# Optimization experiments

Measured on AMD Instinct MI355X. Metric: run time of the kernel, lower is better.

The kernel has to match this reference:

```python
import jax, jax.numpy as jnp
import numpy as np

IN_DIM = 1024
OUT_DIM = 1024
QK_DIM = OUT_DIM // 4  # 256


def setup_inputs() -> dict:
    key = jax.random.key(0)
    kx, ky, kq, kk, kv = jax.random.split(key, 5)
    B, Sq, Sk = 16, 2048, 2048
    x = jax.random.normal(kx, (B, Sq, IN_DIM), dtype=jnp.float32)
    y = jax.random.normal(ky, (B, Sk, IN_DIM), dtype=jnp.float32)
    s = 1.0 / np.sqrt(IN_DIM)
    Wq = jax.random.normal(kq, (IN_DIM, QK_DIM), dtype=jnp.float32) * s
    Wk = jax.random.normal(kk, (IN_DIM, QK_DIM), dtype=jnp.float32) * s
    Wv = jax.random.normal(kv, (IN_DIM, OUT_DIM), dtype=jnp.float32) * s
    return {"x": x, "y": y, "Wq": Wq, "Wk": Wk, "Wv": Wv}


def reference(x, y, Wq, Wk, Wv):
    # q: [B,Sq,dk], k: [B,Sk,dk]
    q = jnp.einsum("bsd,dk->bsk", x, Wq)
    k = jnp.einsum("btd,dk->btk", y, Wk)
    # NOTE: original scales by out_dim**0.5, not qk dim
    scores = jnp.einsum("bsk,btk->bst", q, k) / jnp.sqrt(jnp.float32(OUT_DIM))
    attn = jax.nn.softmax(scores, axis=-1)
    v = jnp.einsum("btd,de->bte", y, Wv)
    out = jnp.einsum("bst,bte->bse", attn, v)
    return out + x
```

## Files before the change

kernel.cpp:

```cpp
#include <hip/hip_runtime.h>

typedef __attribute__((ext_vector_type(8))) short bf16x8;
typedef __attribute__((ext_vector_type(4))) short s16x4;
typedef __attribute__((ext_vector_type(4))) float f32x4;

#define MFMA16(a,b,c) __builtin_amdgcn_mfma_f32_16x16x32_bf16((a),(b),(c),0,0,0)

__device__ __forceinline__ unsigned short f2bf(float f) {
  unsigned int u = __float_as_uint(f);
  return (unsigned short)((u + 0x7fffu + ((u >> 16) & 1u)) >> 16);
}
__device__ __forceinline__ float bf2f(unsigned short u) {
  return __uint_as_float(((unsigned int)u) << 16);
}

__device__ __forceinline__ void gload16(const void* g, void* l) {
  __builtin_amdgcn_global_load_lds((const __attribute__((address_space(1))) void*)g,
                                   (__attribute__((address_space(3))) void*)l, 16, 0, 0);
}

__global__ __launch_bounds__(256) void cvt_bf16(const float* __restrict__ in,
                                                unsigned short* __restrict__ out, int n8) {
  for (int i = blockIdx.x * 256 + threadIdx.x; i < n8; i += gridDim.x * 256) {
    float4 a = ((const float4*)in)[2 * i];
    float4 b = ((const float4*)in)[2 * i + 1];
    s16x4 p0, p1;
    p0[0] = f2bf(a.x); p0[1] = f2bf(a.y); p0[2] = f2bf(a.z); p0[3] = f2bf(a.w);
    p1[0] = f2bf(b.x); p1[1] = f2bf(b.y); p1[2] = f2bf(b.z); p1[3] = f2bf(b.w);
    ((s16x4*)out)[2 * i] = p0;
    ((s16x4*)out)[2 * i + 1] = p1;
  }
}

__global__ __launch_bounds__(256) void tcvt(const float* __restrict__ W,
                                            unsigned short* __restrict__ Wt, int K, int N) {
  __shared__ float t[32][33];
  const int n0 = blockIdx.x * 32, k0 = blockIdx.y * 32;
  const int c = threadIdx.x & 31, r8 = threadIdx.x >> 5;
#pragma unroll
  for (int p = 0; p < 4; ++p) {
    int r = r8 + p * 8;
    t[r][c] = W[(size_t)(k0 + r) * N + n0 + c];
  }
  __syncthreads();
#pragma unroll
  for (int p = 0; p < 4; ++p) {
    int r = r8 + p * 8;
    Wt[(size_t)(n0 + r) * K + k0 + c] = f2bf(t[c][r]);
  }
}

#define SBAR  do { __builtin_amdgcn_s_barrier(); __builtin_amdgcn_sched_barrier(0); } while (0)

template<int NT, int NTIL, int MODE>
__global__ __launch_bounds__(512) void gemm4p(
    const unsigned short* __restrict__ Aall, const unsigned short* __restrict__ Ball,
    size_t abatch, size_t bbatch, int lda, int ldb,
    unsigned short* __restrict__ Cb, int b0, int nb)
{
  __shared__ __align__(16) unsigned short lds[65536];
  const int bid = blockIdx.x;
  const int bloc = bid % nb, tl = bid / nb;
  const int mtile = tl / NTIL, ntile = tl % NTIL;
  const int gb = b0 + bloc;
  const unsigned short* Ag = Aall + (MODE == 0 ? (size_t)gb : (size_t)bloc) * abatch
                                  + (size_t)mtile * 256 * lda;
  const unsigned short* Bg = Ball + (size_t)gb * bbatch + (size_t)ntile * 256 * ldb;

  const int tid = threadIdx.x, lane = tid & 63, w = tid >> 6;
  const int wm = w >> 2, wn = w & 3;
  const int lrow = lane & 15, lg = lane >> 4;
  char* lb = (char*)lds;

  auto stageU = [&](const unsigned short* G, int ld, int kofs, int ubyte) {
#pragma unroll
    for (int i = 0; i < 2; ++i) {
      int c = tid + 512 * i;
      int row = c >> 2, q = c & 3;
      int qs = q ^ ((row >> 1) & 3);
      gload16(G + (size_t)row * ld + kofs + qs * 8, lb + ubyte + c * 16);
    }
  };
  auto rdfrag = [&](int ubyte, int row) -> bf16x8 {
    return *(const bf16x8*)(lb + ubyte + row * 64 + ((lg ^ ((row >> 1) & 3)) << 4));
  };

  f32x4 acc[8][4] = {};
  bf16x8 afA[4], afB[4], bfrA[4], bfrB[4];

  stageU(Ag, lda, 0,  (0 * 2 + 0) * 16384);
  stageU(Bg, ldb, 0,  (1 * 2 + 0) * 16384);
  stageU(Ag, lda, 32, (2 * 2 + 0) * 16384);
  stageU(Bg, ldb, 32, (3 * 2 + 0) * 16384);
  stageU(Ag, lda, 64, (0 * 2 + 1) * 16384);
  stageU(Bg, ldb, 64, (1 * 2 + 1) * 16384);
  asm volatile("s_waitcnt vmcnt(8)" ::: "memory");
  SBAR;
#pragma unroll
  for (int i = 0; i < 4; ++i) afA[i] = rdfrag(0, wm * 128 + i * 16 + lrow);
#pragma unroll
  for (int nf = 0; nf < 4; ++nf) bfrA[nf] = rdfrag(2 * 16384, wn * 64 + nf * 16 + lrow);

  for (int T = 0; T < NT; ++T) {
    const int pc = T & 1, pn = (T + 1) & 1;
    const int a1b = (2 * 2 + pc) * 16384, b1b = (3 * 2 + pc) * 16384;
    const int a0b = (0 * 2 + pc) * 16384;
    const int t1 = (T + 1 < NT) ? T + 1 : 0;
    const int t2 = (T + 2 < NT) ? T + 2 : 0;

#pragma unroll
    for (int i = 0; i < 4; ++i) afB[i] = rdfrag(a0b, wm * 128 + (i + 4) * 16 + lrow);
    stageU(Ag, lda, t1 * 64 + 32, (2 * 2 + pn) * 16384);
    asm volatile("s_waitcnt lgkmcnt(4)" ::: "memory");
    __builtin_amdgcn_sched_barrier(0);
    __builtin_amdgcn_s_setprio(1);
#pragma unroll
    for (int mf = 0; mf < 4; ++mf)
#pragma unroll
      for (int nf = 0; nf < 4; ++nf)
        acc[mf][nf] = MFMA16(afA[mf], bfrA[nf], acc[mf][nf]);
    __builtin_amdgcn_s_setprio(0);
    asm volatile("s_waitcnt vmcnt(6)" ::: "memory");
    SBAR;

#pragma unroll
    for (int i = 0; i < 4; ++i) afA[i] = rdfrag(a1b, wm * 128 + i * 16 + lrow);
#pragma unroll
    for (int nf = 0; nf < 4; ++nf) bfrB[nf] = rdfrag(b1b, wn * 64 + nf * 16 + lrow);
    stageU(Bg, ldb, t1 * 64 + 32, (3 * 2 + pn) * 16384);
    asm volatile("s_waitcnt lgkmcnt(8)" ::: "memory");
    __builtin_amdgcn_sched_barrier(0);
    __builtin_amdgcn_s_setprio(1);
#pragma unroll
    for (int mf = 0; mf < 4; ++mf)
#pragma unroll
      for (int nf = 0; nf < 4; ++nf)
        acc[mf + 4][nf] = MFMA16(afB[mf], bfrA[nf], acc[mf + 4][nf]);
    __builtin_amdgcn_s_setprio(0);
    SBAR;

#pragma unroll
    for (int i = 0; i < 4; ++i) afB[i] = rdfrag(a1b, wm * 128 + (i + 4) * 16 + lrow);
    stageU(Ag, lda, t2 * 64, (0 * 2 + pc) * 16384);
    asm volatile("s_waitcnt lgkmcnt(4)" ::: "memory");
    __builtin_amdgcn_sched_barrier(0);
    __builtin_amdgcn_s_setprio(1);
#pragma unroll
    for (int mf = 0; mf < 4; ++mf)
#pragma unroll
      for (int nf = 0; nf < 4; ++nf)
        acc[mf][nf] = MFMA16(afA[mf], bfrB[nf], acc[mf][nf]);
    __builtin_amdgcn_s_setprio(0);
    asm volatile("s_waitcnt vmcnt(6)" ::: "memory");
    SBAR;

#pragma unroll
    for (int i = 0; i < 4; ++i) afA[i] = rdfrag((0 * 2 + pn) * 16384, wm * 128 + i * 16 + lrow);
#pragma unroll
    for (int nf = 0; nf < 4; ++nf) bfrA[nf] = rdfrag((1 * 2 + pn) * 16384, wn * 64 + nf * 16 + lrow);
    stageU(Bg, ldb, t2 * 64, (1 * 2 + pc) * 16384);
    asm volatile("s_waitcnt lgkmcnt(8)" ::: "memory");
    __builtin_amdgcn_sched_barrier(0);
    __builtin_amdgcn_s_setprio(1);
#pragma unroll
    for (int mf = 0; mf < 4; ++mf)
#pragma unroll
      for (int nf = 0; nf < 4; ++nf)
        acc[mf + 4][nf] = MFMA16(afB[mf], bfrB[nf], acc[mf + 4][nf]);
    __builtin_amdgcn_s_setprio(0);
    SBAR;
  }

  if (MODE == 0) {
    unsigned short* Cp = Cb + (size_t)bloc * 2048 * 2048;
#pragma unroll
    for (int mf = 0; mf < 8; ++mf)
#pragma unroll
      for (int r = 0; r < 4; ++r) {
        int row = mtile * 256 + wm * 128 + mf * 16 + lg * 4 + r;
#pragma unroll
        for (int nf = 0; nf < 4; ++nf) {
          int col = ntile * 256 + wn * 64 + nf * 16 + lrow;
          Cp[(size_t)row * 2048 + col] = f2bf(acc[mf][nf][r]);
        }
      }
  } else if (MODE == 2) {
    unsigned char* C8 = (unsigned char*)Cb;
#pragma unroll
    for (int mf = 0; mf < 8; ++mf) {
      int m0 = mtile * 256 + wm * 128 + mf * 16 + lg * 4;
      int bb = m0 >> 11, t = m0 & 2047;
      int tw = t >> 6, t64 = t & 63;
#pragma unroll
      for (int nf = 0; nf < 4; ++nf) {
        int e = ntile * 256 + wn * 64 + nf * 16 + lrow;
        int eg = e >> 4;
        int pk = 0;
        pk = __builtin_amdgcn_cvt_pk_fp8_f32(acc[mf][nf][0], acc[mf][nf][1], pk, false);
        pk = __builtin_amdgcn_cvt_pk_fp8_f32(acc[mf][nf][2], acc[mf][nf][3], pk, true);
        *(unsigned int*)(C8 + (size_t)bb * 2097152
                            + ((size_t)(eg * 32 + tw)) * 1024 + lrow * 64 + t64)
            = (unsigned int)pk;
      }
    }
  } else {
    unsigned short* Cp = Cb + (size_t)bloc * 16 * 2048 * 256;
    const float scale = (bloc == 0) ? 0.03125f : 1.0f;
#pragma unroll
    for (int mf = 0; mf < 8; ++mf)
#pragma unroll
      for (int r = 0; r < 4; ++r) {
        int row = mtile * 256 + wm * 128 + mf * 16 + lg * 4 + r;
#pragma unroll
        for (int nf = 0; nf < 4; ++nf) {
          int col = wn * 64 + nf * 16 + lrow;
          Cp[(size_t)row * 256 + col] = f2bf(acc[mf][nf][r] * scale);
        }
      }
  }
}

__global__ __launch_bounds__(256) void softmax_kernel(
    const unsigned short* __restrict__ Sp, unsigned char* __restrict__ Pp) {
  const int row = blockIdx.x * 4 + (threadIdx.x >> 6);
  const int lane = threadIdx.x & 63;
  const unsigned short* rp = Sp + (size_t)row * 2048;
  bf16x8 raw[4];
#pragma unroll
  for (int c = 0; c < 4; ++c) raw[c] = *(const bf16x8*)(rp + c * 512 + lane * 8);
  float v[32];
#pragma unroll
  for (int c = 0; c < 4; ++c)
#pragma unroll
    for (int j = 0; j < 8; ++j) v[c * 8 + j] = bf2f((unsigned short)raw[c][j]);
  float mx = v[0];
#pragma unroll
  for (int j = 1; j < 32; ++j) mx = fmaxf(mx, v[j]);
  mx = fmaxf(mx, __shfl_xor(mx, 1));
  mx = fmaxf(mx, __shfl_xor(mx, 2));
  mx = fmaxf(mx, __shfl_xor(mx, 4));
  mx = fmaxf(mx, __shfl_xor(mx, 8));
  mx = fmaxf(mx, __shfl_xor(mx, 16));
  mx = fmaxf(mx, __shfl_xor(mx, 32));
  float sum = 0.f;
#pragma unroll
  for (int j = 0; j < 32; ++j) { v[j] = __expf(v[j] - mx); sum += v[j]; }
  sum += __shfl_xor(sum, 1);
  sum += __shfl_xor(sum, 2);
  sum += __shfl_xor(sum, 4);
  sum += __shfl_xor(sum, 8);
  sum += __shfl_xor(sum, 16);
  sum += __shfl_xor(sum, 32);
  const float scale = 64.0f / sum;
  unsigned char* rp8 = Pp + (size_t)row * 2048;
#pragma unroll
  for (int c = 0; c < 4; ++c) {
    int lo = 0, hi = 0;
    lo = __builtin_amdgcn_cvt_pk_fp8_f32(v[c * 8 + 0] * scale, v[c * 8 + 1] * scale, lo, false);
    lo = __builtin_amdgcn_cvt_pk_fp8_f32(v[c * 8 + 2] * scale, v[c * 8 + 3] * scale, lo, true);
    hi = __builtin_amdgcn_cvt_pk_fp8_f32(v[c * 8 + 4] * scale, v[c * 8 + 5] * scale, hi, false);
    hi = __builtin_amdgcn_cvt_pk_fp8_f32(v[c * 8 + 6] * scale, v[c * 8 + 7] * scale, hi, true);
    uint2 o; o.x = (unsigned int)lo; o.y = (unsigned int)hi;
    *(uint2*)(rp8 + c * 512 + lane * 8) = o;
  }
}

__global__ __launch_bounds__(512) void pvf8_kernel(
    const unsigned char* __restrict__ Pp,
    const unsigned char* __restrict__ Vp,
    const float* __restrict__ X, float* __restrict__ Out,
    int b0, int nb)
{
  __shared__ __align__(16) unsigned char lds[4][16384];
  const int bloc = blockIdx.x % nb, tl = blockIdx.x / nb;
  const int mtile = tl >> 3, ntile = tl & 7;
  const int gb = b0 + bloc;
  const unsigned char* Ag = Pp + (size_t)bloc * 4194304 + (size_t)mtile * 256 * 2048;
  const unsigned char* Vb = Vp + (size_t)gb * 2097152;
  const int NT = 32;
  const int tid = threadIdx.x, lane = tid & 63, w = tid >> 6;
  const int wm = w >> 2, wn = w & 3;
  const int lrow = lane & 15, lg = lane >> 4;

  auto stageA = [&](int jt) {
    unsigned char* dst = lds[jt & 3];
#pragma unroll
    for (int i = 0; i < 2; ++i) {
      int c = tid + 512 * i; int row = c >> 2; int q = (c & 3) ^ ((row >> 1) & 3);
      gload16(Ag + (size_t)row * 2048 + jt * 64 + q * 16, dst + c * 16);
    }
  };
  auto loadB = [&](int jt, long2* bv) {
#pragma unroll
    for (int nf = 0; nf < 2; ++nf) {
      int eg = ntile * 8 + wn * 2 + nf;
      bv[nf] = *(const long2*)(Vb + ((size_t)(eg * 32 + jt)) * 1024 + lrow * 64 + lg * 16);
    }
  };

  f32x4 acc[8][2] = {};
  stageA(0); stageA(1); stageA(2);
  long2 bvc[2];
  loadB(0, bvc);
  asm volatile("s_waitcnt vmcnt(6)" ::: "memory");
  __builtin_amdgcn_sched_barrier(0);

  for (int jt = 0; jt < NT; ++jt) {
    __builtin_amdgcn_s_barrier();
    if (jt + 3 < NT) stageA(jt + 3);
    long2 bvn[2];
    loadB(jt + 1 < NT ? jt + 1 : 0, bvn);
    const unsigned char* Ab = lds[jt & 3];
    {
      long2 av[4];
#pragma unroll
      for (int mf = 0; mf < 4; ++mf) {
        int row = wm * 128 + mf * 16 + lrow;
        av[mf] = *(const long2*)(Ab + row * 64 + ((lg ^ ((row >> 1) & 3)) << 4));
      }
      __builtin_amdgcn_s_setprio(1);
#pragma unroll
      for (int mf = 0; mf < 4; ++mf)
#pragma unroll
        for (int nf = 0; nf < 2; ++nf) {
          acc[mf][nf] = __builtin_amdgcn_mfma_f32_16x16x32_fp8_fp8(av[mf].x, bvc[nf].x, acc[mf][nf], 0, 0, 0);
          acc[mf][nf] = __builtin_amdgcn_mfma_f32_16x16x32_fp8_fp8(av[mf].y, bvc[nf].y, acc[mf][nf], 0, 0, 0);
        }
      __builtin_amdgcn_s_setprio(0);
    }
    {
      long2 av[4];
#pragma unroll
      for (int mf = 0; mf < 4; ++mf) {
        int row = wm * 128 + (mf + 4) * 16 + lrow;
        av[mf] = *(const long2*)(Ab + row * 64 + ((lg ^ ((row >> 1) & 3)) << 4));
      }
      __builtin_amdgcn_s_setprio(1);
#pragma unroll
      for (int mf = 0; mf < 4; ++mf)
#pragma unroll
        for (int nf = 0; nf < 2; ++nf) {
          acc[mf + 4][nf] = __builtin_amdgcn_mfma_f32_16x16x32_fp8_fp8(av[mf].x, bvc[nf].x, acc[mf + 4][nf], 0, 0, 0);
          acc[mf + 4][nf] = __builtin_amdgcn_mfma_f32_16x16x32_fp8_fp8(av[mf].y, bvc[nf].y, acc[mf + 4][nf], 0, 0, 0);
        }
      __builtin_amdgcn_s_setprio(0);
    }
    bvc[0] = bvn[0]; bvc[1] = bvn[1];
  }

#pragma unroll
  for (int mf = 0; mf < 8; ++mf)
#pragma unroll
    for (int r = 0; r < 4; ++r) {
      int row = mtile * 256 + wm * 128 + mf * 16 + lg * 4 + r;
      const float* xr = X   + ((size_t)gb * 2048 + row) * 1024;
      float*      orp = Out + ((size_t)gb * 2048 + row) * 1024;
#pragma unroll
      for (int nf = 0; nf < 2; ++nf) {
        int col = ntile * 128 + wn * 32 + nf * 16 + lrow;
        orp[col] = acc[mf][nf][r] * 0.015625f + xr[col];
      }
    }
}

extern "C" void kernel_launch(void* const* d_in, const int* in_sizes, int n_in,
                              void* d_out, int out_size, void* d_ws, size_t ws_size,
                              hipStream_t stream) {
  (void)in_sizes; (void)n_in; (void)out_size;
  const float* x  = (const float*)d_in[0];
  const float* y  = (const float*)d_in[1];
  const float* Wq = (const float*)d_in[2];
  const float* Wk = (const float*)d_in[3];
  const float* Wv = (const float*)d_in[4];
  float* out = (float*)d_out;

  unsigned short* xb = (unsigned short*)d_out;
  unsigned short* yb = xb + (size_t)16 * 2048 * 1024;

  char* p = (char*)d_ws;
  unsigned short* Wqt = (unsigned short*)p;  p += (size_t)256 * 1024 * 2;
  unsigned short* Wkt = (unsigned short*)p;  p += (size_t)256 * 1024 * 2;
  unsigned short* Wvt = (unsigned short*)p;  p += (size_t)1024 * 1024 * 2;
  unsigned short* qws = (unsigned short*)p;  p += (size_t)16 * 2048 * 256 * 2;
  unsigned short* kws = (unsigned short*)p;  p += (size_t)16 * 2048 * 256 * 2;
  unsigned char*  vp8 = (unsigned char*)p;   p += (size_t)16 * 1024 * 2048;
  char* dyn = p;
  const size_t fixed_bytes = (size_t)(dyn - (char*)d_ws);
  const size_t per_batch = (size_t)2048 * 2048 * 2 + (size_t)2048 * 2048;
  int nb = 1;
  if      (ws_size >= fixed_bytes + 16 * per_batch) nb = 16;
  else if (ws_size >= fixed_bytes + 8  * per_batch) nb = 8;
  else if (ws_size >= fixed_bytes + 4  * per_batch) nb = 4;
  else if (ws_size >= fixed_bytes + 2  * per_batch) nb = 2;
  else nb = 1;
  unsigned short* Sp = (unsigned short*)dyn;
  unsigned char*  Pp = (unsigned char*)(dyn + (size_t)nb * 2048 * 2048 * 2);

  const int n8 = (16 * 2048 * 1024) / 8;
  cvt_bf16<<<2048, 256, 0, stream>>>(x, xb, n8);
  cvt_bf16<<<2048, 256, 0, stream>>>(y, yb, n8);
  tcvt<<<dim3(8, 32),  256, 0, stream>>>(Wq, Wqt, 1024, 256);
  tcvt<<<dim3(8, 32),  256, 0, stream>>>(Wk, Wkt, 1024, 256);
  tcvt<<<dim3(32, 32), 256, 0, stream>>>(Wv, Wvt, 1024, 1024);

  gemm4p<16, 1, 3><<<256, 512, 0, stream>>>(
      xb, Wqt, (size_t)16 * 2048 * 1024, (size_t)256 * 1024, 1024, 1024,
      qws, 0, 2);
  gemm4p<16, 4, 2><<<512, 512, 0, stream>>>(
      yb, Wvt, 0, 0, 1024, 1024, (unsigned short*)vp8, 0, 1);

  for (int b0 = 0; b0 < 16; b0 += nb) {
    gemm4p<4, 8, 0><<<nb * 64, 512, 0, stream>>>(
        qws, kws, (size_t)2048 * 256, (size_t)2048 * 256, 256, 256,
        Sp, b0, nb);
    softmax_kernel<<<nb * 512, 256, 0, stream>>>(Sp, Pp);
    pvf8_kernel<<<nb * 64, 512, 0, stream>>>(Pp, vp8, x, out, b0, nb);
  }
}
```

Before: 430.0 us.

## Merge prologue conversion launches, drop B prefetch in PV kernel, split PV launch

Merges the two activation bf16 conversion kernels into one launch and the three weight transpose-convert kernels into one 3D-grid launch, removing several small launches. In the fp8 PV kernel, the register double-buffered B-operand prefetch is replaced by a same-iteration load, and the initial wait is relaxed. The s_setprio calls become a template option. When all 16 batches fit, the PV launch is split into two halves, the second without priority raising. This trades launch overhead and register pressure against less latency hiding on the B loads.

```diff
diff --git a/kernel.cpp b/kernel.cpp
--- a/kernel.cpp
+++ b/kernel.cpp
@@ -19,23 +19,36 @@
                                    (__attribute__((address_space(3))) void*)l, 16, 0, 0);
 }
 
-__global__ __launch_bounds__(256) void cvt_bf16(const float* __restrict__ in,
-                                                unsigned short* __restrict__ out, int n8) {
-  for (int i = blockIdx.x * 256 + threadIdx.x; i < n8; i += gridDim.x * 256) {
+__global__ __launch_bounds__(256) void cvt_bf16_2(const float* __restrict__ inx,
+                                                  unsigned short* __restrict__ outx,
+                                                  const float* __restrict__ iny,
+                                                  unsigned short* __restrict__ outy,
+                                                  int n8) {
+  const float* in = (blockIdx.x < 2048) ? inx : iny;
+  unsigned short* out = (blockIdx.x < 2048) ? outx : outy;
+  const int b = blockIdx.x & 2047;
+  for (int i = b * 256 + threadIdx.x; i < n8; i += 2048 * 256) {
     float4 a = ((const float4*)in)[2 * i];
-    float4 b = ((const float4*)in)[2 * i + 1];
+    float4 c = ((const float4*)in)[2 * i + 1];
     s16x4 p0, p1;
     p0[0] = f2bf(a.x); p0[1] = f2bf(a.y); p0[2] = f2bf(a.z); p0[3] = f2bf(a.w);
-    p1[0] = f2bf(b.x); p1[1] = f2bf(b.y); p1[2] = f2bf(b.z); p1[3] = f2bf(b.w);
+    p1[0] = f2bf(c.x); p1[1] = f2bf(c.y); p1[2] = f2bf(c.z); p1[3] = f2bf(c.w);
     ((s16x4*)out)[2 * i] = p0;
     ((s16x4*)out)[2 * i + 1] = p1;
   }
 }
 
-__global__ __launch_bounds__(256) void tcvt(const float* __restrict__ W,
-                                            unsigned short* __restrict__ Wt, int K, int N) {
+__global__ __launch_bounds__(256) void tcvt3(const float* __restrict__ Wq, unsigned short* __restrict__ Wqt,
+                                             const float* __restrict__ Wk, unsigned short* __restrict__ Wkt,
+                                             const float* __restrict__ Wv, unsigned short* __restrict__ Wvt) {
   __shared__ float t[32][33];
+  const int which = blockIdx.z;
+  const float* W = which == 0 ? Wq : (which == 1 ? Wk : Wv);
+  unsigned short* Wt = which == 0 ? Wqt : (which == 1 ? Wkt : Wvt);
+  const int N = (which == 2) ? 1024 : 256;
+  const int K = 1024;
   const int n0 = blockIdx.x * 32, k0 = blockIdx.y * 32;
+  if (n0 >= N) return;
   const int c = threadIdx.x & 31, r8 = threadIdx.x >> 5;
 #pragma unroll
   for (int p = 0; p < 4; ++p) {
@@ -265,6 +278,7 @@
   }
 }
 
+template<int PRIO>
 __global__ __launch_bounds__(512) void pvf8_kernel(
     const unsigned char* __restrict__ Pp,
     const unsigned char* __restrict__ Vp,
@@ -290,26 +304,20 @@
       gload16(Ag + (size_t)row * 2048 + jt * 64 + q * 16, dst + c * 16);
     }
   };
-  auto loadB = [&](int jt, long2* bv) {
+
+  f32x4 acc[8][2] = {};
+  stageA(0); stageA(1); stageA(2);
+  asm volatile("s_waitcnt vmcnt(4)" ::: "memory");
+
+  for (int jt = 0; jt < NT; ++jt) {
+    __builtin_amdgcn_s_barrier();
+    long2 bv[2];
 #pragma unroll
     for (int nf = 0; nf < 2; ++nf) {
       int eg = ntile * 8 + wn * 2 + nf;
       bv[nf] = *(const long2*)(Vb + ((size_t)(eg * 32 + jt)) * 1024 + lrow * 64 + lg * 16);
     }
-  };
-
-  f32x4 acc[8][2] = {};
-  stageA(0); stageA(1); stageA(2);
-  long2 bvc[2];
-  loadB(0, bvc);
-  asm volatile("s_waitcnt vmcnt(6)" ::: "memory");
-  __builtin_amdgcn_sched_barrier(0);
-
-  for (int jt = 0; jt < NT; ++jt) {
-    __builtin_amdgcn_s_barrier();
     if (jt + 3 < NT) stageA(jt + 3);
-    long2 bvn[2];
-    loadB(jt + 1 < NT ? jt + 1 : 0, bvn);
     const unsigned char* Ab = lds[jt & 3];
     {
       long2 av[4];
@@ -318,15 +326,15 @@
         int row = wm * 128 + mf * 16 + lrow;
         av[mf] = *(const long2*)(Ab + row * 64 + ((lg ^ ((row >> 1) & 3)) << 4));
       }
-      __builtin_amdgcn_s_setprio(1);
+      if (PRIO) __builtin_amdgcn_s_setprio(1);
 #pragma unroll
       for (int mf = 0; mf < 4; ++mf)
 #pragma unroll
         for (int nf = 0; nf < 2; ++nf) {
-          acc[mf][nf] = __builtin_amdgcn_mfma_f32_16x16x32_fp8_fp8(av[mf].x, bvc[nf].x, acc[mf][nf], 0, 0, 0);
-          acc[mf][nf] = __builtin_amdgcn_mfma_f32_16x16x32_fp8_fp8(av[mf].y, bvc[nf].y, acc[mf][nf], 0, 0, 0);
+          acc[mf][nf] = __builtin_amdgcn_mfma_f32_16x16x32_fp8_fp8(av[mf].x, bv[nf].x, acc[mf][nf], 0, 0, 0);
+          acc[mf][nf] = __builtin_amdgcn_mfma_f32_16x16x32_fp8_fp8(av[mf].y, bv[nf].y, acc[mf][nf], 0, 0, 0);
         }
-      __builtin_amdgcn_s_setprio(0);
+      if (PRIO) __builtin_amdgcn_s_setprio(0);
     }
     {
       long2 av[4];
@@ -335,17 +343,16 @@
         int row = wm * 128 + (mf + 4) * 16 + lrow;
         av[mf] = *(const long2*)(Ab + row * 64 + ((lg ^ ((row >> 1) & 3)) << 4));
       }
-      __builtin_amdgcn_s_setprio(1);
+      if (PRIO) __builtin_amdgcn_s_setprio(1);
 #pragma unroll
       for (int mf = 0; mf < 4; ++mf)
 #pragma unroll
         for (int nf = 0; nf < 2; ++nf) {
-          acc[mf + 4][nf] = __builtin_amdgcn_mfma_f32_16x16x32_fp8_fp8(av[mf].x, bvc[nf].x, acc[mf + 4][nf], 0, 0, 0);
-          acc[mf + 4][nf] = __builtin_amdgcn_mfma_f32_16x16x32_fp8_fp8(av[mf].y, bvc[nf].y, acc[mf + 4][nf], 0, 0, 0);
+          acc[mf + 4][nf] = __builtin_amdgcn_mfma_f32_16x16x32_fp8_fp8(av[mf].x, bv[nf].x, acc[mf + 4][nf], 0, 0, 0);
+          acc[mf + 4][nf] = __builtin_amdgcn_mfma_f32_16x16x32_fp8_fp8(av[mf].y, bv[nf].y, acc[mf + 4][nf], 0, 0, 0);
         }
-      __builtin_amdgcn_s_setprio(0);
-    }
-    bvc[0] = bvn[0]; bvc[1] = bvn[1];
+      if (PRIO) __builtin_amdgcn_s_setprio(0);
+    }
   }
 
 #pragma unroll
@@ -397,11 +404,8 @@
   unsigned char*  Pp = (unsigned char*)(dyn + (size_t)nb * 2048 * 2048 * 2);
 
   const int n8 = (16 * 2048 * 1024) / 8;
-  cvt_bf16<<<2048, 256, 0, stream>>>(x, xb, n8);
-  cvt_bf16<<<2048, 256, 0, stream>>>(y, yb, n8);
-  tcvt<<<dim3(8, 32),  256, 0, stream>>>(Wq, Wqt, 1024, 256);
-  tcvt<<<dim3(8, 32),  256, 0, stream>>>(Wk, Wkt, 1024, 256);
-  tcvt<<<dim3(32, 32), 256, 0, stream>>>(Wv, Wvt, 1024, 1024);
+  cvt_bf16_2<<<4096, 256, 0, stream>>>(x, xb, y, yb, n8);
+  tcvt3<<<dim3(32, 32, 3), 256, 0, stream>>>(Wq, Wqt, Wk, Wkt, Wv, Wvt);
 
   gemm4p<16, 1, 3><<<256, 512, 0, stream>>>(
       xb, Wqt, (size_t)16 * 2048 * 1024, (size_t)256 * 1024, 1024, 1024,
@@ -414,6 +418,11 @@
         qws, kws, (size_t)2048 * 256, (size_t)2048 * 256, 256, 256,
         Sp, b0, nb);
     softmax_kernel<<<nb * 512, 256, 0, stream>>>(Sp, Pp);
-    pvf8_kernel<<<nb * 64, 512, 0, stream>>>(Pp, vp8, x, out, b0, nb);
-  }
-}
+    if (nb == 16) {
+      pvf8_kernel<1><<<8 * 64, 512, 0, stream>>>(Pp, vp8, x, out, 0, 8);
+      pvf8_kernel<0><<<8 * 64, 512, 0, stream>>>(Pp + (size_t)8 * 4194304, vp8, x, out, 8, 8);
+    } else {
+      pvf8_kernel<1><<<nb * 64, 512, 0, stream>>>(Pp, vp8, x, out, b0, nb);
+    }
+  }
+}
```

Measured after the change: 433.5 us. Within noise of the previous version (+0.8%).
